# Kernel tuning notes

Hardware: AMD Instinct MI355X
Metric: run time of the kernel (lower is better)

The kernel has to match this reference:

```python
import jax, jax.numpy as jnp
import numpy as np

NUM_HEADS = 16
HIDDEN = 1024
HEAD = HIDDEN // NUM_HEADS


def setup_inputs() -> dict:
    key = jax.random.key(0)
    k1, k2, k3, k4, k5 = jax.random.split(key, 5)
    b, s, d = 2, 2048, HIDDEN
    scale = 1.0 / np.sqrt(d)
    return {
        "features": jax.random.normal(k1, (b, s, d), dtype=jnp.float32),
        "qkv_w": jax.random.normal(k2, (3 * d, d), dtype=jnp.float32) * scale,  # torch Linear weight [out,in]
        "qkv_b": jax.random.normal(k3, (3 * d,), dtype=jnp.float32) * 0.01,
        "out_w": jax.random.normal(k4, (d, d), dtype=jnp.float32) * scale,
        "out_b": jax.random.normal(k5, (d,), dtype=jnp.float32) * 0.01,
        "use_causal_mask": 0,
    }


def reference(features, qkv_w, qkv_b, out_w, out_b, use_causal_mask):
    b, s, d = features.shape
    qkv = features @ qkv_w.T + qkv_b                      # [b,s,3d]
    q, k, v = jnp.split(qkv, 3, axis=-1)
    # [b,s,d] -> [b,h,s,hd]
    def heads(x):
        return x.reshape(b, s, NUM_HEADS, HEAD).transpose(0, 2, 1, 3)
    q, k, v = heads(q), heads(k), heads(v)
    scores = jnp.einsum("bhqd,bhkd->bhqk", q, k) / np.sqrt(HEAD)
    if use_causal_mask:
        mask = jnp.triu(jnp.ones((s, s), dtype=bool), k=1)
        scores = jnp.where(mask, -jnp.inf, scores)
    attn = jax.nn.softmax(scores, axis=-1)
    out = jnp.einsum("bhqk,bhkd->bhqd", attn, v)          # [b,h,s,hd]
    out = out.transpose(0, 2, 1, 3).reshape(b, s, d)
    return out @ out_w.T + out_b
```

## Files before the change

### kernel.cpp

```cpp
#include <hip/hip_runtime.h>
#include <math.h>

#define BATCH 2
#define SEQ   2048
#define HID   1024
#define NHEAD 16
#define ROWS  (BATCH*SEQ)
#define QKV_N (3*HID)

#define Q_SCALE 0.18033688011112042f
#define SM_SHIFT 8.0f

typedef __attribute__((ext_vector_type(8))) short bf16x8;
typedef __attribute__((ext_vector_type(4))) float f32x4;

__device__ __forceinline__ unsigned short f2b(float f) {
    unsigned u = __float_as_uint(f);
    u += 0x7FFF + ((u >> 16) & 1);
    return (unsigned short)(u >> 16);
}
__device__ __forceinline__ unsigned short f2b_fast(float f) {
    return (unsigned short)((__float_as_uint(f) + 0x8000u) >> 16);
}

#define GLOAD_LDS16(gp, lp) \
    __builtin_amdgcn_global_load_lds((const __attribute__((address_space(1))) void*)(gp), \
                                     (__attribute__((address_space(3))) void*)(lp), 16, 0, 0)

__global__ __launch_bounds__(256)
void cvt_all(const float* __restrict__ a, unsigned short* __restrict__ oa, int na4,
             const float* __restrict__ b, unsigned short* __restrict__ ob, int nb4,
             const float* __restrict__ c, unsigned short* __restrict__ oc, int nc4) {
    int i = blockIdx.x * 256 + threadIdx.x;
    const float* src; unsigned short* dst; int j;
    if (i < na4)            { src = a; dst = oa; j = i; }
    else if (i < na4 + nb4) { src = b; dst = ob; j = i - na4; }
    else if (i < na4 + nb4 + nc4) { src = c; dst = oc; j = i - na4 - nb4; }
    else return;
    float4 v = reinterpret_cast<const float4*>(src)[j];
    ushort4 o;
    o.x = f2b(v.x); o.y = f2b(v.y); o.z = f2b(v.z); o.w = f2b(v.w);
    reinterpret_cast<ushort4*>(dst)[j] = o;
}

template<int MODE>
__global__ __launch_bounds__(256)
void gemm_mfma(const unsigned short* __restrict__ A, const unsigned short* __restrict__ B,
               const float* __restrict__ bias, void* __restrict__ Cout,
               unsigned short* __restrict__ vt, int M, int N, int K) {
    __shared__ unsigned short As[128 * 32];
    __shared__ unsigned short Bs[128 * 32];
    const int tid = threadIdx.x;
    const int w = tid >> 6, l = tid & 63;
    const int wm = w >> 1, wn = w & 1;
    const int l15 = l & 15, l4 = l >> 4;
    const long row0 = (long)blockIdx.y * 128;
    const long col0 = (long)blockIdx.x * 128;

    f32x4 acc[4][4];
    #pragma unroll
    for (int m = 0; m < 4; ++m)
        #pragma unroll
        for (int n = 0; n < 4; ++n) acc[m][n] = (f32x4)0.0f;

    const int lr   = l >> 2;
    const int slot = (l & 3) ^ (lr & 3);

    for (int k0 = 0; k0 < K; k0 += 32) {
        __syncthreads();
        #pragma unroll
        for (int c = 0; c < 2; ++c) {
            int r = w * 32 + c * 16 + lr;
            GLOAD_LDS16(A + (row0 + r) * K + k0 + slot * 8, As + (w * 32 + c * 16) * 32);
            GLOAD_LDS16(B + (col0 + r) * K + k0 + slot * 8, Bs + (w * 32 + c * 16) * 32);
        }
        __syncthreads();

        bf16x8 af[4], bfr[4];
        #pragma unroll
        for (int m = 0; m < 4; ++m) {
            int row = wm * 64 + m * 16 + l15;
            af[m] = *(const bf16x8*)((const char*)As + row * 64 + ((l4 ^ (row & 3)) << 4));
        }
        #pragma unroll
        for (int n = 0; n < 4; ++n) {
            int row = wn * 64 + n * 16 + l15;
            bfr[n] = *(const bf16x8*)((const char*)Bs + row * 64 + ((l4 ^ (row & 3)) << 4));
        }
        #pragma unroll
        for (int m = 0; m < 4; ++m)
            #pragma unroll
            for (int n = 0; n < 4; ++n)
                acc[m][n] = __builtin_amdgcn_mfma_f32_16x16x32_bf16(af[m], bfr[n], acc[m][n], 0, 0, 0);
    }

    #pragma unroll
    for (int m = 0; m < 4; ++m) {
        #pragma unroll
        for (int n = 0; n < 4; ++n) {
            long ccol = col0 + wn * 64 + n * 16 + l15;
            float bv = bias[ccol];
            #pragma unroll
            for (int r2 = 0; r2 < 4; ++r2) {
                long crow = row0 + wm * 64 + m * 16 + l4 * 4 + r2;
                float v = acc[m][n][r2] + bv;
                if (MODE == 0) {
                    ((float*)Cout)[crow * N + ccol] = v;
                } else {
                    if (ccol < 1024) {
                        ((unsigned short*)Cout)[crow * QKV_N + ccol] = f2b(v * Q_SCALE);
                    } else if (ccol < 2048) {
                        ((unsigned short*)Cout)[crow * QKV_N + ccol] = f2b(v);
                    } else {
                        long cc = ccol - 2048;
                        long h = cc >> 6, d = cc & 63;
                        long b = crow >> 11, s = crow & 2047;
                        vt[(((b * NHEAD + h) * 64 + d) << 11) + s] = f2b(v);
                    }
                }
            }
        }
    }
}

__global__ __launch_bounds__(256)
void attn_mfma(const unsigned short* __restrict__ qkv, const unsigned short* __restrict__ vt,
               unsigned short* __restrict__ attno, const int* __restrict__ use_mask) {
    __shared__ unsigned short Ks [64 * 64];
    __shared__ unsigned short Vts[64 * 64];
    __shared__ unsigned short Ps [4 * 16 * 64];
    const int tid = threadIdx.x;
    const int w = tid >> 6, l = tid & 63;
    const int l15 = l & 15, l4 = l >> 4;
    const int bid  = blockIdx.x;
    const int orig = (bid & 7) * 128 + (bid >> 3);
    const int qt = orig & 31, bh = orig >> 5;
    const int b = bh >> 4, h = bh & 15;
    const int q0 = qt * 64;
    const int causal = use_mask[0];
    const int NT = causal ? (qt + 1) : (SEQ / 64);

    bf16x8 qf[2];
    {
        const unsigned short* qp = qkv + (size_t)(b * SEQ + q0 + w * 16 + l15) * QKV_N + h * 64;
        qf[0] = *(const bf16x8*)(qp + l4 * 8);
        qf[1] = *(const bf16x8*)(qp + 32 + l4 * 8);
    }

    f32x4 o_acc[4];
    #pragma unroll
    for (int n = 0; n < 4; ++n) o_acc[n] = (f32x4)0.0f;
    float l_r[4] = {0.f, 0.f, 0.f, 0.f};

    const int srow = l >> 3, g = l & 7;
    const int r0   = w * 16 + srow;
    const int wso  = (g ^ srow) << 3;
    const unsigned short* kbase = qkv + (size_t)b * SEQ * QKV_N + HID + h * 64;
    const unsigned short* vbase = vt + (size_t)bh * 64 * SEQ;
    unsigned short* pw = Ps + w * 1024;

    bf16x8 kreg[2], vreg[2];
    #pragma unroll
    for (int c = 0; c < 2; ++c) {
        kreg[c] = *(const bf16x8*)(kbase + (size_t)(r0 + c * 8) * QKV_N + g * 8);
        vreg[c] = *(const bf16x8*)(vbase + (size_t)(r0 + c * 8) * SEQ + g * 8);
    }

    for (int kt = 0; kt < NT; ++kt) {
        __syncthreads();
        #pragma unroll
        for (int c = 0; c < 2; ++c) {
            *(bf16x8*)(Ks  + (r0 + c * 8) * 64 + wso) = kreg[c];
            *(bf16x8*)(Vts + (r0 + c * 8) * 64 + wso) = vreg[c];
        }
        __syncthreads();

        if (kt + 1 < NT) {
            int nk0 = (kt + 1) * 64;
            #pragma unroll
            for (int c = 0; c < 2; ++c) {
                kreg[c] = *(const bf16x8*)(kbase + (size_t)(nk0 + r0 + c * 8) * QKV_N + g * 8);
                vreg[c] = *(const bf16x8*)(vbase + (size_t)(r0 + c * 8) * SEQ + nk0 + g * 8);
            }
        }

        f32x4 s_acc[4];
        #pragma unroll
        for (int n = 0; n < 4; ++n) s_acc[n] = (f32x4)0.0f;
        #pragma unroll
        for (int ks = 0; ks < 2; ++ks) {
            #pragma unroll
            for (int n = 0; n < 4; ++n) {
                int row = n * 16 + l15;
                bf16x8 kf = *(const bf16x8*)((const char*)Ks + row * 128 + (((ks * 4 + l4) ^ (row & 7)) << 4));
                s_acc[n] = __builtin_amdgcn_mfma_f32_16x16x32_bf16(qf[ks], kf, s_acc[n], 0, 0, 0);
            }
        }
        if (causal) {
            int kk0 = kt * 64;
            #pragma unroll
            for (int n = 0; n < 4; ++n)
                #pragma unroll
                for (int r2 = 0; r2 < 4; ++r2) {
                    int col  = kk0 + n * 16 + l15;
                    int rowq = q0 + w * 16 + l4 * 4 + r2;
                    if (col > rowq) s_acc[n][r2] = -INFINITY;
                }
        }

        #pragma unroll
        for (int n = 0; n < 4; ++n) {
            #pragma unroll
            for (int r2 = 0; r2 < 4; ++r2) {
                float p = exp2f(s_acc[n][r2] - SM_SHIFT);
                l_r[r2] += p;
                int prow = l4 * 4 + r2;
                int pofs = (n * 16 + l15) * 2;
                *(unsigned short*)((char*)pw + prow * 128 + (pofs ^ ((prow & 7) << 4))) = f2b_fast(p);
            }
        }

        #pragma unroll
        for (int ks = 0; ks < 2; ++ks) {
            bf16x8 pf = *(const bf16x8*)((const char*)pw + l15 * 128 + (((ks * 4 + l4) ^ (l15 & 7)) << 4));
            #pragma unroll
            for (int n = 0; n < 4; ++n) {
                int vrow = n * 16 + l15;
                bf16x8 vf = *(const bf16x8*)((const char*)Vts + vrow * 128 + (((ks * 4 + l4) ^ (vrow & 7)) << 4));
                o_acc[n] = __builtin_amdgcn_mfma_f32_16x16x32_bf16(pf, vf, o_acc[n], 0, 0, 0);
            }
        }
    }

    #pragma unroll
    for (int r2 = 0; r2 < 4; ++r2) {
        float t = l_r[r2];
        #pragma unroll
        for (int off = 1; off < 16; off <<= 1) t += __shfl_xor(t, off);
        float inv = 1.0f / t;
        size_t orow = (size_t)(b * SEQ + q0 + w * 16 + l4 * 4 + r2);
        #pragma unroll
        for (int n = 0; n < 4; ++n)
            attno[orow * HID + h * 64 + n * 16 + l15] = f2b(o_acc[n][r2] * inv);
    }
}

extern "C" void kernel_launch(void* const* d_in, const int* in_sizes, int n_in,
                              void* d_out, int out_size, void* d_ws, size_t ws_size,
                              hipStream_t stream) {
    const float* features = (const float*)d_in[0];
    const float* qkv_w    = (const float*)d_in[1];
    const float* qkv_b    = (const float*)d_in[2];
    const float* out_w    = (const float*)d_in[3];
    const float* out_b    = (const float*)d_in[4];
    const int*   use_mask = (const int*)d_in[5];

    char* ws = (char*)d_ws;
    unsigned short* fbf     = (unsigned short*)(ws);
    unsigned short* wbf     = (unsigned short*)(ws + 8388608);
    unsigned short* owbf    = (unsigned short*)(ws + 14680064);
    unsigned short* qkvbf   = (unsigned short*)(ws + 16777216);
    unsigned short* vtbuf   = (unsigned short*)(ws + 41943040);
    unsigned short* attnobf = (unsigned short*)(ws + 50331648);

    cvt_all<<<8192, 256, 0, stream>>>(features, fbf, 1048576,
                                      qkv_w, wbf, 786432,
                                      out_w, owbf, 262144);

    dim3 g1(QKV_N / 128, ROWS / 128);
    gemm_mfma<2><<<g1, 256, 0, stream>>>(fbf, wbf, qkv_b, (void*)qkvbf, vtbuf,
                                         ROWS, QKV_N, HID);

    attn_mfma<<<1024, 256, 0, stream>>>(qkvbf, vtbuf, attnobf, use_mask);

    dim3 g3(HID / 128, ROWS / 128);
    gemm_mfma<0><<<g3, 256, 0, stream>>>(attnobf, owbf, out_b, d_out, (unsigned short*)nullptr,
                                         ROWS, HID, HID);
}
```

Baseline: 159.2 us.

## Enlarge attention query tile to 128 rows and compute row sums via MFMA

Each attention block now handles 128 queries (32 per wave, two MFMA row tiles), so every K/V tile loaded into LDS is reused across twice as many queries and the grid halves to 512 blocks. QK^T is computed transposed (K as the A operand) so P can be written to LDS as packed 4-element stores instead of scalar 16-bit stores. Softmax row sums move from per-lane scalar adds plus a shuffle reduction to an MFMA against a ones vector. The fixed exp shift is removed and P rounding switches to round-to-nearest-even. The cost is more registers per wave, fewer blocks for occupancy, and reliance on unshifted exponentials of the scaled scores staying in range.

```diff
diff --git a/kernel.cpp b/kernel.cpp
--- a/kernel.cpp
+++ b/kernel.cpp
@@ -9,7 +9,6 @@
 #define QKV_N (3*HID)
 
 #define Q_SCALE 0.18033688011112042f
-#define SM_SHIFT 8.0f
 
 typedef __attribute__((ext_vector_type(8))) short bf16x8;
 typedef __attribute__((ext_vector_type(4))) float f32x4;
@@ -19,8 +18,8 @@
     u += 0x7FFF + ((u >> 16) & 1);
     return (unsigned short)(u >> 16);
 }
-__device__ __forceinline__ unsigned short f2b_fast(float f) {
-    return (unsigned short)((__float_as_uint(f) + 0x8000u) >> 16);
+__device__ __forceinline__ unsigned pk2(float a, float b) {
+    return (unsigned)f2b(a) | ((unsigned)f2b(b) << 16);
 }
 
 #define GLOAD_LDS16(gp, lp) \
@@ -48,8 +47,8 @@
 void gemm_mfma(const unsigned short* __restrict__ A, const unsigned short* __restrict__ B,
                const float* __restrict__ bias, void* __restrict__ Cout,
                unsigned short* __restrict__ vt, int M, int N, int K) {
-    __shared__ unsigned short As[128 * 32];
-    __shared__ unsigned short Bs[128 * 32];
+    __shared__ __align__(16) unsigned short As[128 * 32];
+    __shared__ __align__(16) unsigned short Bs[128 * 32];
     const int tid = threadIdx.x;
     const int w = tid >> 6, l = tid & 63;
     const int wm = w >> 1, wn = w & 1;
@@ -126,38 +125,46 @@
 __global__ __launch_bounds__(256)
 void attn_mfma(const unsigned short* __restrict__ qkv, const unsigned short* __restrict__ vt,
                unsigned short* __restrict__ attno, const int* __restrict__ use_mask) {
-    __shared__ unsigned short Ks [64 * 64];
-    __shared__ unsigned short Vts[64 * 64];
-    __shared__ unsigned short Ps [4 * 16 * 64];
+    __shared__ __align__(16) unsigned short Ks [64 * 64];
+    __shared__ __align__(16) unsigned short Vts[64 * 64];
+    __shared__ __align__(16) unsigned short Ps [4][32 * 64];
     const int tid = threadIdx.x;
     const int w = tid >> 6, l = tid & 63;
     const int l15 = l & 15, l4 = l >> 4;
     const int bid  = blockIdx.x;
-    const int orig = (bid & 7) * 128 + (bid >> 3);
-    const int qt = orig & 31, bh = orig >> 5;
+    const int orig = (bid & 7) * 64 + (bid >> 3);
+    const int qt = orig & 15, bh = orig >> 4;
     const int b = bh >> 4, h = bh & 15;
-    const int q0 = qt * 64;
+    const int q0 = qt * 128;
+    const int wq0 = q0 + w * 32;
     const int causal = use_mask[0];
-    const int NT = causal ? (qt + 1) : (SEQ / 64);
-
-    bf16x8 qf[2];
-    {
-        const unsigned short* qp = qkv + (size_t)(b * SEQ + q0 + w * 16 + l15) * QKV_N + h * 64;
-        qf[0] = *(const bf16x8*)(qp + l4 * 8);
-        qf[1] = *(const bf16x8*)(qp + 32 + l4 * 8);
-    }
-
-    f32x4 o_acc[4];
-    #pragma unroll
-    for (int n = 0; n < 4; ++n) o_acc[n] = (f32x4)0.0f;
-    float l_r[4] = {0.f, 0.f, 0.f, 0.f};
+    const int NT = causal ? 2 * (qt + 1) : (SEQ / 64);
+
+    bf16x8 qf[2][2];
+    #pragma unroll
+    for (int m = 0; m < 2; ++m) {
+        const unsigned short* qp = qkv + (size_t)(b * SEQ + wq0 + m * 16 + l15) * QKV_N + h * 64;
+        qf[m][0] = *(const bf16x8*)(qp + l4 * 8);
+        qf[m][1] = *(const bf16x8*)(qp + 32 + l4 * 8);
+    }
+
+    f32x4 o_acc[2][4];
+    #pragma unroll
+    for (int m = 0; m < 2; ++m)
+        #pragma unroll
+        for (int n = 0; n < 4; ++n) o_acc[m][n] = (f32x4)0.0f;
+    f32x4 l_acc[2] = {(f32x4)0.0f, (f32x4)0.0f};
+
+    bf16x8 ones;
+    #pragma unroll
+    for (int j = 0; j < 8; ++j) ones[j] = (short)0x3F80;
 
     const int srow = l >> 3, g = l & 7;
     const int r0   = w * 16 + srow;
     const int wso  = (g ^ srow) << 3;
     const unsigned short* kbase = qkv + (size_t)b * SEQ * QKV_N + HID + h * 64;
     const unsigned short* vbase = vt + (size_t)bh * 64 * SEQ;
-    unsigned short* pw = Ps + w * 1024;
+    unsigned short* pw = Ps[w];
 
     bf16x8 kreg[2], vreg[2];
     #pragma unroll
@@ -184,16 +191,20 @@
             }
         }
 
-        f32x4 s_acc[4];
-        #pragma unroll
-        for (int n = 0; n < 4; ++n) s_acc[n] = (f32x4)0.0f;
+        f32x4 s_acc[4][2];
+        #pragma unroll
+        for (int n = 0; n < 4; ++n)
+            #pragma unroll
+            for (int m = 0; m < 2; ++m) s_acc[n][m] = (f32x4)0.0f;
         #pragma unroll
         for (int ks = 0; ks < 2; ++ks) {
             #pragma unroll
             for (int n = 0; n < 4; ++n) {
                 int row = n * 16 + l15;
                 bf16x8 kf = *(const bf16x8*)((const char*)Ks + row * 128 + (((ks * 4 + l4) ^ (row & 7)) << 4));
-                s_acc[n] = __builtin_amdgcn_mfma_f32_16x16x32_bf16(qf[ks], kf, s_acc[n], 0, 0, 0);
+                #pragma unroll
+                for (int m = 0; m < 2; ++m)
+                    s_acc[n][m] = __builtin_amdgcn_mfma_f32_16x16x32_bf16(kf, qf[m][ks], s_acc[n][m], 0, 0, 0);
             }
         }
         if (causal) {
@@ -201,47 +212,62 @@
             #pragma unroll
             for (int n = 0; n < 4; ++n)
                 #pragma unroll
-                for (int r2 = 0; r2 < 4; ++r2) {
-                    int col  = kk0 + n * 16 + l15;
-                    int rowq = q0 + w * 16 + l4 * 4 + r2;
-                    if (col > rowq) s_acc[n][r2] = -INFINITY;
-                }
-        }
-
-        #pragma unroll
-        for (int n = 0; n < 4; ++n) {
-            #pragma unroll
-            for (int r2 = 0; r2 < 4; ++r2) {
-                float p = exp2f(s_acc[n][r2] - SM_SHIFT);
-                l_r[r2] += p;
-                int prow = l4 * 4 + r2;
-                int pofs = (n * 16 + l15) * 2;
-                *(unsigned short*)((char*)pw + prow * 128 + (pofs ^ ((prow & 7) << 4))) = f2b_fast(p);
+                for (int m = 0; m < 2; ++m)
+                    #pragma unroll
+                    for (int r2 = 0; r2 < 4; ++r2) {
+                        int krow = kk0 + n * 16 + l4 * 4 + r2;
+                        int qcol = wq0 + m * 16 + l15;
+                        if (krow > qcol) s_acc[n][m][r2] = -INFINITY;
+                    }
+        }
+
+        #pragma unroll
+        for (int m = 0; m < 2; ++m) {
+            int prow = m * 16 + l15;
+            #pragma unroll
+            for (int n = 0; n < 4; ++n) {
+                float p0 = exp2f(s_acc[n][m][0]);
+                float p1 = exp2f(s_acc[n][m][1]);
+                float p2 = exp2f(s_acc[n][m][2]);
+                float p3 = exp2f(s_acc[n][m][3]);
+                uint2 pk;
+                pk.x = pk2(p0, p1);
+                pk.y = pk2(p2, p3);
+                int byteoff = (n * 32 + l4 * 8) ^ ((prow & 7) << 4);
+                *(uint2*)((char*)pw + prow * 128 + byteoff) = pk;
             }
         }
 
         #pragma unroll
         for (int ks = 0; ks < 2; ++ks) {
-            bf16x8 pf = *(const bf16x8*)((const char*)pw + l15 * 128 + (((ks * 4 + l4) ^ (l15 & 7)) << 4));
+            bf16x8 pf[2];
+            #pragma unroll
+            for (int m = 0; m < 2; ++m) {
+                int row = m * 16 + l15;
+                pf[m] = *(const bf16x8*)((const char*)pw + row * 128 + (((ks * 4 + l4) ^ (row & 7)) << 4));
+                l_acc[m] = __builtin_amdgcn_mfma_f32_16x16x32_bf16(pf[m], ones, l_acc[m], 0, 0, 0);
+            }
             #pragma unroll
             for (int n = 0; n < 4; ++n) {
                 int vrow = n * 16 + l15;
                 bf16x8 vf = *(const bf16x8*)((const char*)Vts + vrow * 128 + (((ks * 4 + l4) ^ (vrow & 7)) << 4));
-                o_acc[n] = __builtin_amdgcn_mfma_f32_16x16x32_bf16(pf, vf, o_acc[n], 0, 0, 0);
-            }
-        }
-    }
-
-    #pragma unroll
-    for (int r2 = 0; r2 < 4; ++r2) {
-        float t = l_r[r2];
-        #pragma unroll
-        for (int off = 1; off < 16; off <<= 1) t += __shfl_xor(t, off);
-        float inv = 1.0f / t;
-        size_t orow = (size_t)(b * SEQ + q0 + w * 16 + l4 * 4 + r2);
-        #pragma unroll
-        for (int n = 0; n < 4; ++n)
-            attno[orow * HID + h * 64 + n * 16 + l15] = f2b(o_acc[n][r2] * inv);
+                #pragma unroll
+                for (int m = 0; m < 2; ++m)
+                    o_acc[m][n] = __builtin_amdgcn_mfma_f32_16x16x32_bf16(pf[m], vf, o_acc[m][n], 0, 0, 0);
+            }
+        }
+    }
+
+    #pragma unroll
+    for (int m = 0; m < 2; ++m) {
+        #pragma unroll
+        for (int r2 = 0; r2 < 4; ++r2) {
+            float inv = 1.0f / l_acc[m][r2];
+            size_t orow = (size_t)(b * SEQ + wq0 + m * 16 + l4 * 4 + r2);
+            #pragma unroll
+            for (int n = 0; n < 4; ++n)
+                attno[orow * HID + h * 64 + n * 16 + l15] = f2b(o_acc[m][n][r2] * inv);
+        }
     }
 }
 
@@ -271,7 +297,7 @@
     gemm_mfma<2><<<g1, 256, 0, stream>>>(fbf, wbf, qkv_b, (void*)qkvbf, vtbuf,
                                          ROWS, QKV_N, HID);
 
-    attn_mfma<<<1024, 256, 0, stream>>>(qkvbf, vtbuf, attnobf, use_mask);
+    attn_mfma<<<512, 256, 0, stream>>>(qkvbf, vtbuf, attnobf, use_mask);
 
     dim3 g3(HID / 128, ROWS / 128);
     gemm_mfma<0><<<g3, 256, 0, stream>>>(attnobf, owbf, out_b, d_out, (unsigned short*)nullptr,
```

After: 156.0 us. -2.0%, faster.
